# Optimization experiments

Measured on AMD Instinct MI355X. Metric: run time of the kernel, lower is better.

The kernel has to match this reference:

```python
import jax, jax.numpy as jnp
import numpy as np

HEADS = 8


def setup_inputs() -> dict:
    key = jax.random.key(0)
    ks = jax.random.split(key, 7)
    b, t, e, h = 4, 2048, 128, HEADS
    x = jax.random.normal(ks[0], (b, t, e), dtype=jnp.float32)
    mask = jax.random.randint(ks[1], (1, t, t), 0, 2, dtype=jnp.int32)
    Wq = jax.random.normal(ks[2], (e, e * h), dtype=jnp.float32) / np.sqrt(e)
    Wk = jax.random.normal(ks[3], (e, e * h), dtype=jnp.float32) / np.sqrt(e)
    Wv = jax.random.normal(ks[4], (e, e * h), dtype=jnp.float32) / np.sqrt(e)
    Wu = jax.random.normal(ks[5], (e * h, e), dtype=jnp.float32) / np.sqrt(e * h)
    bu = jax.random.normal(ks[6], (e,), dtype=jnp.float32) * 0.01
    return {"x": x, "mask": mask, "Wq": Wq, "Wk": Wk, "Wv": Wv, "Wu": Wu, "bu": bu}


def reference(x, mask, Wq, Wk, Wv, Wu, bu):
    b, t, e = x.shape
    h = HEADS
    scale = e ** (-0.25)  # original scales q and k each by e**(1/4)
    # project and split heads: (b, t, h, e) -> (b, h, t, e)
    q = (x @ Wq).reshape(b, t, h, e).transpose(0, 2, 1, 3) * scale
    k = (x @ Wk).reshape(b, t, h, e).transpose(0, 2, 1, 3) * scale
    v = (x @ Wv).reshape(b, t, h, e).transpose(0, 2, 1, 3)
    dot = jnp.einsum('bhqe,bhke->bhqk', q, k)  # (b, h, t, t)
    # causal mask: strictly-upper triangle set to -inf (mask_diagonal=False -> offset=1)
    causal = jnp.triu(jnp.ones((t, t), dtype=bool), k=1)
    dot = jnp.where(causal, jnp.float32(-np.inf), dot)
    # external mask: positions where mask == 0 set to -1e9 (broadcast over b*h)
    dot = jnp.where((mask == 0)[:, None, :, :], jnp.float32(-1e9), dot)
    att = jax.nn.softmax(dot, axis=-1)
    out = jnp.einsum('bhqk,bhke->bhqe', att, v)
    out = out.transpose(0, 2, 1, 3).reshape(b, t, h * e)
    return out @ Wu + bu
```

## Files before the change

kernel.cpp:

```cpp
#include <hip/hip_runtime.h>
#include <hip/hip_bf16.h>

typedef unsigned short u16;
typedef unsigned int u32;
typedef __attribute__((ext_vector_type(8))) short bf16x8;
typedef __attribute__((ext_vector_type(4))) float f32x4;
typedef __attribute__((ext_vector_type(8))) unsigned short u16x8;
typedef __attribute__((ext_vector_type(2))) unsigned int u32x2;

#define T_ 2048
#define H_ 8
#define BH_ 32
#define M_ 8192
#define SCALE_QK 0.29730177875068026f

__device__ __forceinline__ u16 f2bf(float f) {
  union { __hip_bfloat16 h; u16 u; } cv; cv.h = __float2bfloat16(f); return cv.u;
}
__device__ __forceinline__ float bf2f(u16 u) {
  union { u16 u; __hip_bfloat16 h; } cv; cv.u = u; return __bfloat162float(cv.h);
}


__global__ __launch_bounds__(256)
void prep_kernel(const float* __restrict__ x, const float* __restrict__ Wq,
                 const float* __restrict__ Wk, const float* __restrict__ Wv,
                 const float* __restrict__ Wu,
                 u16* __restrict__ xb, u16* __restrict__ WT, u16* __restrict__ WuT)
{
  int i = blockIdx.x * 256 + threadIdx.x;
  if (i < M_ * 128) { xb[i] = f2bf(x[i]); return; }
  int j = i - M_ * 128;
  if (j < 3072 * 128) {
    int n = j >> 7, k = j & 127;
    float w;
    if (n < 1024)      w = Wq[k * 1024 + n] * SCALE_QK;
    else if (n < 2048) w = Wk[k * 1024 + (n - 1024)] * SCALE_QK;
    else               w = Wv[k * 1024 + (n - 2048)];
    WT[j] = f2bf(w);
    return;
  }
  int u = j - 3072 * 128;
  if (u < 128 * 1024) {
    int n = u >> 10, k = u & 1023;
    WuT[u] = f2bf(Wu[k * 128 + n]);
  }
}

__global__ __launch_bounds__(256)
void maskprep_kernel(const int* __restrict__ mask, u32* __restrict__ mbits,
                     u32* __restrict__ deglist, u32* __restrict__ degcount,
                     float* __restrict__ cnt0inv)
{
  int wave = threadIdx.x >> 6, lane = threadIdx.x & 63;
  int q = blockIdx.x * 4 + wave;
  const int* row = mask + (long)q * 2048;
  unsigned long long anyvis = 0ull;
  int cnt1 = 0;
  for (int it = 0; it < 32; ++it) {
    int k = it * 64 + lane;
    unsigned long long bal = __ballot(row[k] != 0);
    if (lane == 0) {
      mbits[q * 64 + it * 2]     = (u32)bal;
      mbits[q * 64 + it * 2 + 1] = (u32)(bal >> 32);
    }
    cnt1 += __popcll(bal);
    int lim = q - it * 64;
    if (lim >= 63)      anyvis |= bal;
    else if (lim >= 0)  anyvis |= (bal & ((2ull << lim) - 1ull));
  }
  if (lane == 0) {
    int c0 = 2048 - cnt1;
    cnt0inv[q] = (c0 > 0) ? 1.0f / (float)c0 : 0.0f;
    if (anyvis == 0ull) {
      u32 slot = atomicAdd(degcount, 1u);
      deglist[slot] = (u32)q;
    }
  }
}

__global__ __launch_bounds__(256)
void qkv_kernel(const u16* __restrict__ xb, const u16* __restrict__ WT,
                u16* __restrict__ Qb, u16* __restrict__ Kimg, u16* __restrict__ Vimg)
{
  __shared__ __align__(16) u16 As[128 * 128];
  __shared__ __align__(16) u16 Bs[128 * 128];
  const int tid = threadIdx.x;
  const int n0 = blockIdx.x * 128;
  const int m0 = blockIdx.y * 128;
#pragma unroll
  for (int i = 0; i < 8; ++i) {
    int c = tid + 256 * i;
    int row = c >> 4, d0 = (c & 15) * 8;
    int soff = row * 128 + ((((d0 >> 3)) ^ (row & 15)) << 3);
    *(u16x8*)(&As[soff]) = *(const u16x8*)(&xb[(m0 + row) * 128 + d0]);
    *(u16x8*)(&Bs[soff]) = *(const u16x8*)(&WT[(n0 + row) * 128 + d0]);
  }
  __syncthreads();
  const int wave = tid >> 6, lane = tid & 63;
  const int lr = lane & 15, lg = lane >> 4;
  const int wm = (wave >> 1) * 64, wn = (wave & 1) * 64;
  f32x4 acc[4][4];
#pragma unroll
  for (int a = 0; a < 4; ++a)
#pragma unroll
    for (int b = 0; b < 4; ++b) acc[a][b] = (f32x4){0.f, 0.f, 0.f, 0.f};
#pragma unroll
  for (int ks = 0; ks < 4; ++ks) {
    bf16x8 af[4], bf[4];
#pragma unroll
    for (int mt = 0; mt < 4; ++mt) {
      int row = wm + mt * 16 + lr, chunk = lg + ks * 4;
      af[mt] = *(const bf16x8*)(&As[row * 128 + ((chunk ^ (row & 15)) << 3)]);
    }
#pragma unroll
    for (int nt = 0; nt < 4; ++nt) {
      int row = wn + nt * 16 + lr, chunk = lg + ks * 4;
      bf[nt] = *(const bf16x8*)(&Bs[row * 128 + ((chunk ^ (row & 15)) << 3)]);
    }
#pragma unroll
    for (int mt = 0; mt < 4; ++mt)
#pragma unroll
      for (int nt = 0; nt < 4; ++nt)
        acc[mt][nt] = __builtin_amdgcn_mfma_f32_16x16x32_bf16(af[mt], bf[nt], acc[mt][nt], 0, 0, 0);
  }
  const int mat = n0 >> 10;
  const int hh = (n0 & 1023) >> 7;
  const int bb = m0 >> 11;
  const long bhb = (long)(bb * H_ + hh);
  __syncthreads();
  if (mat != 2) {
#pragma unroll
    for (int mt = 0; mt < 4; ++mt)
#pragma unroll
      for (int nt = 0; nt < 4; ++nt)
#pragma unroll
        for (int r = 0; r < 4; ++r) {
          int tl = wm + mt * 16 + lg * 4 + r;
          int d  = wn + nt * 16 + lr;
          As[tl * 128 + ((((d >> 3)) ^ (tl & 15)) << 3) + (d & 7)] = f2bf(acc[mt][nt][r]);
        }
    __syncthreads();
    if (mat == 0) {
#pragma unroll
      for (int i = 0; i < 8; ++i) {
        int c = tid + 256 * i;
        int row = c >> 4, d0 = (c & 15) * 8;
        u16x8 v = *(const u16x8*)(&As[row * 128 + ((((d0 >> 3)) ^ (row & 15)) << 3)]);
        *(u16x8*)(&Qb[(bhb * T_ + ((m0 + row) & 2047)) * 128 + d0]) = v;
      }
    } else {
#pragma unroll
      for (int i = 0; i < 8; ++i) {
        int c = tid + 256 * i;
        int row = c >> 4, d0 = (c & 15) * 8;
        u16x8 v = *(const u16x8*)(&As[row * 128 + ((((d0 >> 3)) ^ (row & 15)) << 3)]);
        int t = (m0 + row) & 2047;
        int kt = t >> 6, kr = t & 63;
        *(u16x8*)(&Kimg[(bhb * 32 + kt) * 8192 + kr * 128 + ((((d0 >> 3)) ^ (kr & 15)) << 3)]) = v;
      }
    }
  } else {
    u16* TT = As;
#pragma unroll
    for (int mt = 0; mt < 4; ++mt)
#pragma unroll
      for (int nt = 0; nt < 4; ++nt)
#pragma unroll
        for (int r = 0; r < 4; ++r) {
          int tl = wm + mt * 16 + lg * 4 + r;
          int d  = wn + nt * 16 + lr;
          TT[d * 128 + ((((tl >> 3)) ^ (d & 15)) << 3) + (tl & 7)] = f2bf(acc[mt][nt][r]);
        }
    __syncthreads();
    const int tg0 = m0 & 2047;
#pragma unroll
    for (int i = 0; i < 8; ++i) {
      int c = tid + 256 * i;
      int d = c >> 4, t0 = (c & 15) * 8;
      u16x8 v = *(const u16x8*)(&TT[d * 128 + ((((t0 >> 3)) ^ (d & 15)) << 3)]);
      int tg = tg0 + t0;
      int kt = tg >> 6, kk = tg & 63;
      *(u16x8*)(&Vimg[(bhb * 32 + kt) * 8192 + d * 64 + (((kk >> 3) ^ (d & 7)) << 3)]) = v;
    }
  }
}

__global__ __launch_bounds__(256, 3)
void flash_kernel(const u16* __restrict__ Qb, const u16* __restrict__ Kimg,
                  const u16* __restrict__ Vimg, const u32* __restrict__ mbits,
                  u16* __restrict__ Ob)
{
  __shared__ __align__(16) u16 Ks[64 * 128];
  __shared__ __align__(16) u16 VTs[128 * 64];
  __shared__ __align__(16) u16 Ps[4][16 * 64];
  const int tid = threadIdx.x;
  const int qt = 31 - (blockIdx.x >> 5);
  const int bh = blockIdx.x & 31;
  const int q0 = qt * 64;
  const int wave = tid >> 6, lane = tid & 63;
  const int lr = lane & 15, lg = lane >> 4;
  const long base = (long)bh * T_ * 128;
  const long iblk = (long)bh * 32;
  const int ldsoff = wave * 2048 + lane * 8;
  const int qrl = wave * 16 + lr;
  const int swz = (lr & 7) << 1;

  bf16x8 qf[4];
  {
    const u16* qrow = Qb + base + (long)(q0 + qrl) * 128;
#pragma unroll
    for (int ks = 0; ks < 4; ++ks)
      qf[ks] = *(const bf16x8*)(&qrow[lg * 8 + ks * 32]);
  }
  f32x4 acc[8];
#pragma unroll
  for (int i = 0; i < 8; ++i) acc[i] = (f32x4){0.f, 0.f, 0.f, 0.f};
  float mrun = -__builtin_inff(), lrun = 0.f;

  u16x8 kreg[4], vreg[4];
  {
    const u16* ks0 = Kimg + iblk * 8192 + ldsoff;
    const u16* vs0 = Vimg + iblk * 8192 + ldsoff;
#pragma unroll
    for (int i = 0; i < 4; ++i) {
      kreg[i] = *(const u16x8*)(ks0 + i * 512);
      vreg[i] = *(const u16x8*)(vs0 + i * 512);
    }
  }

  for (int kt = 0; kt <= qt; ++kt) {
    __syncthreads();
#pragma unroll
    for (int i = 0; i < 4; ++i) {
      *(u16x8*)(&Ks[ldsoff + i * 512]) = kreg[i];
      *(u16x8*)(&VTs[ldsoff + i * 512]) = vreg[i];
    }
    __syncthreads();
    if (kt < qt) {
      const u16* ksn = Kimg + (iblk + kt + 1) * 8192 + ldsoff;
      const u16* vsn = Vimg + (iblk + kt + 1) * 8192 + ldsoff;
#pragma unroll
      for (int i = 0; i < 4; ++i) {
        kreg[i] = *(const u16x8*)(ksn + i * 512);
        vreg[i] = *(const u16x8*)(vsn + i * 512);
      }
    }
    u32 mw0, mw1;
    {
      const u32* mp = &mbits[(q0 + qrl) * 64 + kt * 2];
      mw0 = mp[0]; mw1 = mp[1];
    }

    f32x4 s[4];
    __builtin_amdgcn_s_setprio(1);
#pragma unroll
    for (int ft = 0; ft < 4; ++ft) {
      f32x4 sa = (f32x4){0.f, 0.f, 0.f, 0.f};
#pragma unroll
      for (int ks = 0; ks < 4; ++ks) {
        int kr = ft * 16 + lr, chunk = lg + ks * 4;
        bf16x8 kf = *(const bf16x8*)(&Ks[kr * 128 + ((chunk ^ (kr & 15)) << 3)]);
        sa = __builtin_amdgcn_mfma_f32_16x16x32_bf16(kf, qf[ks], sa, 0, 0, 0);
      }
      s[ft] = sa;
    }
    __builtin_amdgcn_s_setprio(0);
    const bool diag = (kt == qt);
#pragma unroll
    for (int ft = 0; ft < 4; ++ft) {
      u32 w = (ft & 2) ? mw1 : mw0;
      int kbase = ft * 16 + lg * 4;
      int sh = ((ft & 1) << 4) + lg * 4;
#pragma unroll
      for (int r = 0; r < 4; ++r) {
        bool vis = (w >> (sh + r)) & 1u;
        if (diag && (kbase + r) > qrl) vis = false;
        if (!vis) s[ft][r] = -__builtin_inff();
      }
    }
    float t0 = fmaxf(fmaxf(s[0][0], s[0][1]), fmaxf(s[0][2], s[0][3]));
    float t1 = fmaxf(fmaxf(s[1][0], s[1][1]), fmaxf(s[1][2], s[1][3]));
    float t2 = fmaxf(fmaxf(s[2][0], s[2][1]), fmaxf(s[2][2], s[2][3]));
    float t3 = fmaxf(fmaxf(s[3][0], s[3][1]), fmaxf(s[3][2], s[3][3]));
    float tm = fmaxf(fmaxf(t0, t1), fmaxf(t2, t3));
    tm = fmaxf(tm, __shfl_xor(tm, 16));
    tm = fmaxf(tm, __shfl_xor(tm, 32));
    float mnew = fmaxf(mrun, tm);
    float msafe = (mnew == -__builtin_inff()) ? 0.f : mnew;
    float fac = __expf(mrun - msafe);
    const bool grew = (mnew != mrun);
    mrun = mnew;
    float rs = 0.f;
#pragma unroll
    for (int ft = 0; ft < 4; ++ft) {
      float p0 = __expf(s[ft][0] - msafe), p1 = __expf(s[ft][1] - msafe);
      float p2 = __expf(s[ft][2] - msafe), p3 = __expf(s[ft][3] - msafe);
      s[ft][0] = p0; s[ft][1] = p1; s[ft][2] = p2; s[ft][3] = p3;
      rs += (p0 + p1) + (p2 + p3);
    }
    rs += __shfl_xor(rs, 16);
    rs += __shfl_xor(rs, 32);
    lrun = lrun * fac + rs;
    if (__any(grew)) {
#pragma unroll
      for (int nt = 0; nt < 8; ++nt)
#pragma unroll
        for (int r = 0; r < 4; ++r) acc[nt][r] *= fac;
    }
#pragma unroll
    for (int ft = 0; ft < 4; ++ft) {
      u16 h0 = f2bf(s[ft][0]), h1 = f2bf(s[ft][1]);
      u16 h2 = f2bf(s[ft][2]), h3 = f2bf(s[ft][3]);
      u32x2 pw; pw[0] = (u32)h0 | ((u32)h1 << 16); pw[1] = (u32)h2 | ((u32)h3 << 16);
      int ch4 = (ft * 4 + lg) ^ swz;
      *(u32x2*)(&Ps[wave][lr * 64 + ch4 * 4]) = pw;
    }
    bf16x8 pa[2];
#pragma unroll
    for (int s2 = 0; s2 < 2; ++s2) {
      int ch4b = (s2 * 8 + lg * 2) ^ swz;
      pa[s2] = *(const bf16x8*)(&Ps[wave][lr * 64 + ch4b * 4]);
    }
    __builtin_amdgcn_s_setprio(1);
#pragma unroll
    for (int nt = 0; nt < 8; ++nt)
#pragma unroll
      for (int s2 = 0; s2 < 2; ++s2) {
        int d = nt * 16 + lr, chunk = lg + s2 * 4;
        bf16x8 vf = *(const bf16x8*)(&VTs[d * 64 + ((chunk ^ (d & 7)) << 3)]);
        acc[nt] = __builtin_amdgcn_mfma_f32_16x16x32_bf16(vf, pa[s2], acc[nt], 0, 0, 0);
      }
    __builtin_amdgcn_s_setprio(0);
  }
  const float inv = (lrun > 0.f) ? 1.f / lrun : 0.f;
  const long orow = base + (long)(q0 + qrl) * 128;
#pragma unroll
  for (int nt = 0; nt < 8; ++nt) {
    u16 h0 = f2bf(acc[nt][0] * inv), h1 = f2bf(acc[nt][1] * inv);
    u16 h2 = f2bf(acc[nt][2] * inv), h3 = f2bf(acc[nt][3] * inv);
    u32x2 ow; ow[0] = (u32)h0 | ((u32)h1 << 16); ow[1] = (u32)h2 | ((u32)h3 << 16);
    *(u32x2*)(&Ob[orow + nt * 16 + lg * 4]) = ow;
  }
}

__global__ __launch_bounds__(256)
void fixup_partial_kernel(const u32* __restrict__ deglist, const u32* __restrict__ degcount,
                          const u32* __restrict__ mbits, const u16* __restrict__ Vimg,
                          float* __restrict__ partial)
{
  const int slot = blockIdx.z;
  const u32 cnt = *degcount;
  if (slot >= (int)cnt) return;
  const int ksec = blockIdx.x, bh = blockIdx.y;
  const int q = (int)deglist[slot];
  const int t = threadIdx.x;
  const int d = t & 127, kc = t >> 7;
  const u16* vb = Vimg + ((long)bh * 32 + ksec) * 8192 + d * 64;
  const u32 w0 = mbits[q * 64 + ksec * 2];
  const u32 w1 = mbits[q * 64 + ksec * 2 + 1];
  float a = 0.f;
#pragma unroll
  for (int i = 0; i < 4; ++i) {
    int c = kc * 4 + i;
    u32 bits = ((kc == 0) ? (w0 >> (c * 8)) : (w1 >> ((c - 4) * 8))) & 0xffu;
    u16x8 v = *(const u16x8*)(&vb[(c ^ (d & 7)) << 3]);
#pragma unroll
    for (int j = 0; j < 8; ++j)
      a += ((bits >> j) & 1u) ? 0.f : bf2f(v[j]);
  }
  __shared__ float tmp[2][128];
  tmp[kc][d] = a;
  __syncthreads();
  if (t < 128)
    partial[(((long)slot * BH_ + bh) * 128 + d) * 32 + ksec] = tmp[0][d] + tmp[1][d];
}

__global__ __launch_bounds__(128)
void fixup_combine_kernel(const u32* __restrict__ deglist, const u32* __restrict__ degcount,
                          const float* __restrict__ cnt0inv, const float* __restrict__ partial,
                          u16* __restrict__ Ob)
{
  const int slot = blockIdx.x;
  const u32 cnt = *degcount;
  if (slot >= (int)cnt) return;
  const int bh = blockIdx.y;
  const int q = (int)deglist[slot];
  const int d = threadIdx.x;
  const float* p = partial + (((long)slot * BH_ + bh) * 128 + d) * 32;
  float s = 0.f;
#pragma unroll
  for (int i = 0; i < 8; ++i) {
    f32x4 v = *(const f32x4*)(&p[i * 4]);
    s += (v[0] + v[1]) + (v[2] + v[3]);
  }
  Ob[((long)bh * T_ + q) * 128 + d] = f2bf(s * cnt0inv[q]);
}

__global__ __launch_bounds__(256)
void fixup_slow_kernel(const u32* __restrict__ deglist, const u32* __restrict__ degcount,
                       const float* __restrict__ cnt0inv, const u32* __restrict__ mbits,
                       const u16* __restrict__ Vimg, u16* __restrict__ Ob)
{
  const u32 cnt = *degcount;
  const int bh = blockIdx.y;
  const int d = threadIdx.x & 127, half = threadIdx.x >> 7;
  __shared__ float tmp[2][128];
  const u16* vb = Vimg + (long)bh * 32 * 8192;
  for (u32 idx = 8 + blockIdx.x; idx < cnt; idx += gridDim.x) {
    const int q = (int)deglist[idx];
    const float inv = cnt0inv[q];
    float a = 0.f;
#pragma unroll 16
    for (int i = 0; i < 128; ++i) {
      int k0 = half * 1024 + i * 8;
      u32 w = mbits[q * 64 + (k0 >> 5)];
      u32 bits = (w >> (k0 & 31)) & 0xffu;
      int kt = k0 >> 6, kk = k0 & 63;
      u16x8 v = *(const u16x8*)(&vb[(long)kt * 8192 + d * 64 + (((kk >> 3) ^ (d & 7)) << 3)]);
#pragma unroll
      for (int j = 0; j < 8; ++j)
        a += ((bits >> j) & 1u) ? 0.f : bf2f(v[j]);
    }
    tmp[half][d] = a;
    __syncthreads();
    if (half == 0)
      Ob[((long)bh * T_ + q) * 128 + d] = f2bf((tmp[0][d] + tmp[1][d]) * inv);
    __syncthreads();
  }
}

__global__ __launch_bounds__(256)
void outproj_kernel(const u16* __restrict__ Ob, const u16* __restrict__ WuT,
                    const float* __restrict__ bu, float* __restrict__ out)
{
  __shared__ __align__(16) u16 As[32 * 128];
  __shared__ __align__(16) u16 Bs[128 * 128];
  const int tid = threadIdx.x;
  const int m0 = blockIdx.x * 32;
  const int wave = tid >> 6, lane = tid & 63;
  const int lr = lane & 15, lg = lane >> 4;
  f32x4 acc[2][2];
#pragma unroll
  for (int a = 0; a < 2; ++a)
#pragma unroll
    for (int b = 0; b < 2; ++b) acc[a][b] = (f32x4){0.f, 0.f, 0.f, 0.f};
  for (int kc = 0; kc < 8; ++kc) {
    __syncthreads();
#pragma unroll
    for (int i = 0; i < 2; ++i) {
      int c = tid + 256 * i;
      int row = c >> 4, d0 = (c & 15) * 8;
      int m = m0 + row, bb = m >> 11, t = m & 2047;
      *(u16x8*)(&As[row * 128 + ((((d0 >> 3)) ^ (row & 15)) << 3)]) =
          *(const u16x8*)(&Ob[((long)(bb * H_ + kc) * T_ + t) * 128 + d0]);
    }
#pragma unroll
    for (int i = 0; i < 8; ++i) {
      int c = tid + 256 * i;
      int row = c >> 4, d0 = (c & 15) * 8;
      *(u16x8*)(&Bs[row * 128 + ((((d0 >> 3)) ^ (row & 15)) << 3)]) =
          *(const u16x8*)(&WuT[row * 1024 + kc * 128 + d0]);
    }
    __syncthreads();
#pragma unroll
    for (int ks = 0; ks < 4; ++ks) {
      bf16x8 af[2], bf2[2];
#pragma unroll
      for (int mt = 0; mt < 2; ++mt) {
        int row = mt * 16 + lr, chunk = lg + ks * 4;
        af[mt] = *(const bf16x8*)(&As[row * 128 + ((chunk ^ (row & 15)) << 3)]);
      }
#pragma unroll
      for (int nt = 0; nt < 2; ++nt) {
        int row = wave * 32 + nt * 16 + lr, chunk = lg + ks * 4;
        bf2[nt] = *(const bf16x8*)(&Bs[row * 128 + ((chunk ^ (row & 15)) << 3)]);
      }
#pragma unroll
      for (int mt = 0; mt < 2; ++mt)
#pragma unroll
        for (int nt = 0; nt < 2; ++nt)
          acc[mt][nt] = __builtin_amdgcn_mfma_f32_16x16x32_bf16(af[mt], bf2[nt], acc[mt][nt], 0, 0, 0);
    }
  }
#pragma unroll
  for (int mt = 0; mt < 2; ++mt)
#pragma unroll
    for (int nt = 0; nt < 2; ++nt) {
      int n = wave * 32 + nt * 16 + lr;
      float bias = bu[n];
#pragma unroll
      for (int r = 0; r < 4; ++r) {
        int m = m0 + mt * 16 + lg * 4 + r;
        out[(long)m * 128 + n] = acc[mt][nt][r] + bias;
      }
    }
}

extern "C" void kernel_launch(void* const* d_in, const int* in_sizes, int n_in,
                              void* d_out, int out_size, void* d_ws, size_t ws_size,
                              hipStream_t stream)
{
  (void)in_sizes; (void)n_in; (void)out_size; (void)ws_size;
  const float* x   = (const float*)d_in[0];
  const int*   msk = (const int*)d_in[1];
  const float* Wq  = (const float*)d_in[2];
  const float* Wk  = (const float*)d_in[3];
  const float* Wv  = (const float*)d_in[4];
  const float* Wu  = (const float*)d_in[5];
  const float* bu  = (const float*)d_in[6];
  float* out = (float*)d_out;

  u16* Qb   = (u16*)d_ws;
  u16* Kimg = Qb + (size_t)BH_ * T_ * 128;
  u16* Vimg = Kimg + (size_t)BH_ * T_ * 128;
  u16* Obf  = Vimg + (size_t)BH_ * T_ * 128;
  u16* xb   = Obf + (size_t)BH_ * T_ * 128;
  u16* WT   = xb + (size_t)M_ * 128;
  u16* WuT  = WT + (size_t)3072 * 128;
  u32* mbits   = (u32*)(WuT + (size_t)128 * 1024);
  u32* deglist = mbits + (size_t)2048 * 64;
  u32* degcount = deglist + 2048;
  float* cnt0inv = (float*)(degcount + 1);
  float* partial = (float*)Qb;

  hipMemsetAsync(degcount, 0, sizeof(u32), stream);
  prep_kernel<<<6144, 256, 0, stream>>>(x, Wq, Wk, Wv, Wu, xb, WT, WuT);
  maskprep_kernel<<<512, 256, 0, stream>>>(msk, mbits, deglist, degcount, cnt0inv);
  qkv_kernel<<<dim3(24, 64), 256, 0, stream>>>(xb, WT, Qb, Kimg, Vimg);
  flash_kernel<<<1024, 256, 0, stream>>>(Qb, Kimg, Vimg, mbits, Obf);
  fixup_partial_kernel<<<dim3(32, 32, 8), 256, 0, stream>>>(deglist, degcount, mbits, Vimg, partial);
  fixup_combine_kernel<<<dim3(8, 32), 128, 0, stream>>>(deglist, degcount, cnt0inv, partial, Obf);
  fixup_slow_kernel<<<dim3(32, 32), 256, 0, stream>>>(deglist, degcount, cnt0inv, mbits, Vimg, Obf);
  outproj_kernel<<<256, 256, 0, stream>>>(Obf, WuT, bu, out);
}
```

Before: 135.8 us.

## Use 128-row query tiles with 32x32 MFMA and register-shuffled P operands

The flash kernel now handles 128 query rows per block (32 per wave) and uses 32x32x16 bf16 MFMA for both QK^T and PV, which doubles reuse of each K/V tile loaded into LDS. The probability matrix is repacked into MFMA operands with cross-lane shuffles instead of a round trip through LDS, and the output is staged through LDS for coalesced 16-byte stores. Query-tile scheduling is changed to interleave heavy and light causal tiles. The cost is more registers per thread (occupancy hint lowered from 3 to 2 blocks) and half as many blocks, which may leave the device underfilled.

Measured after the change: 179.0 us. 31.8% more time.

```diff
diff --git a/kernel.cpp b/kernel.cpp
--- a/kernel.cpp
+++ b/kernel.cpp
@@ -5,6 +5,7 @@
 typedef unsigned int u32;
 typedef __attribute__((ext_vector_type(8))) short bf16x8;
 typedef __attribute__((ext_vector_type(4))) float f32x4;
+typedef __attribute__((ext_vector_type(16))) float f32x16;
 typedef __attribute__((ext_vector_type(8))) unsigned short u16x8;
 typedef __attribute__((ext_vector_type(2))) unsigned int u32x2;
 
@@ -186,36 +187,39 @@
   }
 }
 
-__global__ __launch_bounds__(256, 3)
+__global__ __launch_bounds__(256, 2)
 void flash_kernel(const u16* __restrict__ Qb, const u16* __restrict__ Kimg,
                   const u16* __restrict__ Vimg, const u32* __restrict__ mbits,
                   u16* __restrict__ Ob)
 {
-  __shared__ __align__(16) u16 Ks[64 * 128];
-  __shared__ __align__(16) u16 VTs[128 * 64];
-  __shared__ __align__(16) u16 Ps[4][16 * 64];
+  __shared__ __align__(16) u16 SMEM[128 * 128];
+  u16* const Ks  = SMEM;
+  u16* const VTs = SMEM + 8192;
   const int tid = threadIdx.x;
-  const int qt = 31 - (blockIdx.x >> 5);
+  const int idx = blockIdx.x >> 5;
+  const int qt = (idx < 8) ? (15 - idx) : (idx - 8);
   const int bh = blockIdx.x & 31;
-  const int q0 = qt * 64;
+  const int q0 = qt * 128;
   const int wave = tid >> 6, lane = tid & 63;
-  const int lr = lane & 15, lg = lane >> 4;
+  const int l31 = lane & 31, h = lane >> 5;
   const long base = (long)bh * T_ * 128;
   const long iblk = (long)bh * 32;
   const int ldsoff = wave * 2048 + lane * 8;
-  const int qrl = wave * 16 + lr;
-  const int swz = (lr & 7) << 1;
-
-  bf16x8 qf[4];
+  const int qrl = wave * 32 + l31;
+  const int nkv = 2 * (qt + 1);
+
+  bf16x8 qf[8];
   {
-    const u16* qrow = Qb + base + (long)(q0 + qrl) * 128;
-#pragma unroll
-    for (int ks = 0; ks < 4; ++ks)
-      qf[ks] = *(const bf16x8*)(&qrow[lg * 8 + ks * 32]);
-  }
-  f32x4 acc[8];
-#pragma unroll
-  for (int i = 0; i < 8; ++i) acc[i] = (f32x4){0.f, 0.f, 0.f, 0.f};
+    const u16* qrow = Qb + base + (long)(q0 + qrl) * 128 + h * 8;
+#pragma unroll
+    for (int st = 0; st < 8; ++st)
+      qf[st] = *(const bf16x8*)(&qrow[st * 16]);
+  }
+  f32x16 acc[4];
+#pragma unroll
+  for (int i = 0; i < 4; ++i)
+#pragma unroll
+    for (int r = 0; r < 16; ++r) acc[i][r] = 0.f;
   float mrun = -__builtin_inff(), lrun = 0.f;
 
   u16x8 kreg[4], vreg[4];
@@ -229,7 +233,7 @@
     }
   }
 
-  for (int kt = 0; kt <= qt; ++kt) {
+  for (int kt = 0; kt < nkv; ++kt) {
     __syncthreads();
 #pragma unroll
     for (int i = 0; i < 4; ++i) {
@@ -237,7 +241,7 @@
       *(u16x8*)(&VTs[ldsoff + i * 512]) = vreg[i];
     }
     __syncthreads();
-    if (kt < qt) {
+    if (kt + 1 < nkv) {
       const u16* ksn = Kimg + (iblk + kt + 1) * 8192 + ldsoff;
       const u16* vsn = Vimg + (iblk + kt + 1) * 8192 + ldsoff;
 #pragma unroll
@@ -252,95 +256,139 @@
       mw0 = mp[0]; mw1 = mp[1];
     }
 
-    f32x4 s[4];
+    f32x16 s[2];
+#pragma unroll
+    for (int k2 = 0; k2 < 2; ++k2)
+#pragma unroll
+      for (int r = 0; r < 16; ++r) s[k2][r] = 0.f;
     __builtin_amdgcn_s_setprio(1);
 #pragma unroll
-    for (int ft = 0; ft < 4; ++ft) {
-      f32x4 sa = (f32x4){0.f, 0.f, 0.f, 0.f};
-#pragma unroll
-      for (int ks = 0; ks < 4; ++ks) {
-        int kr = ft * 16 + lr, chunk = lg + ks * 4;
-        bf16x8 kf = *(const bf16x8*)(&Ks[kr * 128 + ((chunk ^ (kr & 15)) << 3)]);
-        sa = __builtin_amdgcn_mfma_f32_16x16x32_bf16(kf, qf[ks], sa, 0, 0, 0);
-      }
-      s[ft] = sa;
+    for (int k2 = 0; k2 < 2; ++k2) {
+      const int key = k2 * 32 + l31;
+      const int swk = (key & 15);
+#pragma unroll
+      for (int st = 0; st < 8; ++st) {
+        int chunk = 2 * st + h;
+        bf16x8 kf = *(const bf16x8*)(&Ks[key * 128 + ((chunk ^ swk) << 3)]);
+        s[k2] = __builtin_amdgcn_mfma_f32_32x32x16_bf16(kf, qf[st], s[k2], 0, 0, 0);
+      }
     }
     __builtin_amdgcn_s_setprio(0);
-    const bool diag = (kt == qt);
-#pragma unroll
-    for (int ft = 0; ft < 4; ++ft) {
-      u32 w = (ft & 2) ? mw1 : mw0;
-      int kbase = ft * 16 + lg * 4;
-      int sh = ((ft & 1) << 4) + lg * 4;
-#pragma unroll
-      for (int r = 0; r < 4; ++r) {
-        bool vis = (w >> (sh + r)) & 1u;
-        if (diag && (kbase + r) > qrl) vis = false;
-        if (!vis) s[ft][r] = -__builtin_inff();
-      }
-    }
-    float t0 = fmaxf(fmaxf(s[0][0], s[0][1]), fmaxf(s[0][2], s[0][3]));
-    float t1 = fmaxf(fmaxf(s[1][0], s[1][1]), fmaxf(s[1][2], s[1][3]));
-    float t2 = fmaxf(fmaxf(s[2][0], s[2][1]), fmaxf(s[2][2], s[2][3]));
-    float t3 = fmaxf(fmaxf(s[3][0], s[3][1]), fmaxf(s[3][2], s[3][3]));
-    float tm = fmaxf(fmaxf(t0, t1), fmaxf(t2, t3));
-    tm = fmaxf(tm, __shfl_xor(tm, 16));
+
+    const bool diag = (kt >= 2 * qt);
+    const int kv0 = kt * 64;
+#pragma unroll
+    for (int k2 = 0; k2 < 2; ++k2) {
+      u32 w = k2 ? mw1 : mw0;
+#pragma unroll
+      for (int r = 0; r < 16; ++r) {
+        int bitpos = (r & 3) + 8 * (r >> 2) + 4 * h;
+        bool vis = (w >> bitpos) & 1u;
+        if (diag && (kv0 + k2 * 32 + bitpos) > (q0 + qrl)) vis = false;
+        if (!vis) s[k2][r] = -__builtin_inff();
+      }
+    }
+    float tv[8];
+#pragma unroll
+    for (int i = 0; i < 8; ++i)
+      tv[i] = fmaxf(fmaxf(s[i >> 2][(i & 3) * 4 + 0], s[i >> 2][(i & 3) * 4 + 1]),
+                    fmaxf(s[i >> 2][(i & 3) * 4 + 2], s[i >> 2][(i & 3) * 4 + 3]));
+    float tm = fmaxf(fmaxf(fmaxf(tv[0], tv[1]), fmaxf(tv[2], tv[3])),
+                     fmaxf(fmaxf(tv[4], tv[5]), fmaxf(tv[6], tv[7])));
     tm = fmaxf(tm, __shfl_xor(tm, 32));
     float mnew = fmaxf(mrun, tm);
     float msafe = (mnew == -__builtin_inff()) ? 0.f : mnew;
     float fac = __expf(mrun - msafe);
     const bool grew = (mnew != mrun);
     mrun = mnew;
-    float rs = 0.f;
-#pragma unroll
-    for (int ft = 0; ft < 4; ++ft) {
-      float p0 = __expf(s[ft][0] - msafe), p1 = __expf(s[ft][1] - msafe);
-      float p2 = __expf(s[ft][2] - msafe), p3 = __expf(s[ft][3] - msafe);
-      s[ft][0] = p0; s[ft][1] = p1; s[ft][2] = p2; s[ft][3] = p3;
-      rs += (p0 + p1) + (p2 + p3);
-    }
-    rs += __shfl_xor(rs, 16);
+    float rs0 = 0.f, rs1 = 0.f, rs2 = 0.f, rs3 = 0.f;
+#pragma unroll
+    for (int k2 = 0; k2 < 2; ++k2)
+#pragma unroll
+      for (int g = 0; g < 4; ++g) {
+        float p0 = __expf(s[k2][4 * g + 0] - msafe);
+        float p1 = __expf(s[k2][4 * g + 1] - msafe);
+        float p2 = __expf(s[k2][4 * g + 2] - msafe);
+        float p3 = __expf(s[k2][4 * g + 3] - msafe);
+        s[k2][4 * g + 0] = p0; s[k2][4 * g + 1] = p1;
+        s[k2][4 * g + 2] = p2; s[k2][4 * g + 3] = p3;
+        rs0 += p0; rs1 += p1; rs2 += p2; rs3 += p3;
+      }
+    float rs = (rs0 + rs1) + (rs2 + rs3);
     rs += __shfl_xor(rs, 32);
     lrun = lrun * fac + rs;
     if (__any(grew)) {
 #pragma unroll
-      for (int nt = 0; nt < 8; ++nt)
-#pragma unroll
-        for (int r = 0; r < 4; ++r) acc[nt][r] *= fac;
-    }
-#pragma unroll
-    for (int ft = 0; ft < 4; ++ft) {
-      u16 h0 = f2bf(s[ft][0]), h1 = f2bf(s[ft][1]);
-      u16 h2 = f2bf(s[ft][2]), h3 = f2bf(s[ft][3]);
-      u32x2 pw; pw[0] = (u32)h0 | ((u32)h1 << 16); pw[1] = (u32)h2 | ((u32)h3 << 16);
-      int ch4 = (ft * 4 + lg) ^ swz;
-      *(u32x2*)(&Ps[wave][lr * 64 + ch4 * 4]) = pw;
-    }
-    bf16x8 pa[2];
-#pragma unroll
-    for (int s2 = 0; s2 < 2; ++s2) {
-      int ch4b = (s2 * 8 + lg * 2) ^ swz;
-      pa[s2] = *(const bf16x8*)(&Ps[wave][lr * 64 + ch4b * 4]);
+      for (int dt = 0; dt < 4; ++dt)
+#pragma unroll
+        for (int r = 0; r < 16; ++r) acc[dt][r] *= fac;
+    }
+    u32x2 grp[2][4];
+#pragma unroll
+    for (int k2 = 0; k2 < 2; ++k2)
+#pragma unroll
+      for (int g = 0; g < 4; ++g) {
+        u16 b0 = f2bf(s[k2][4 * g + 0]), b1 = f2bf(s[k2][4 * g + 1]);
+        u16 b2 = f2bf(s[k2][4 * g + 2]), b3 = f2bf(s[k2][4 * g + 3]);
+        grp[k2][g][0] = (u32)b0 | ((u32)b1 << 16);
+        grp[k2][g][1] = (u32)b2 | ((u32)b3 << 16);
+      }
+    u32x2 rcv[2][2];
+#pragma unroll
+    for (int k2 = 0; k2 < 2; ++k2)
+#pragma unroll
+      for (int e = 0; e < 2; ++e) {
+        u32x2 snd = h ? grp[k2][e * 2] : grp[k2][e * 2 + 1];
+        rcv[k2][e][0] = (u32)__shfl_xor((int)snd[0], 32);
+        rcv[k2][e][1] = (u32)__shfl_xor((int)snd[1], 32);
+      }
+    bf16x8 pa[4];
+#pragma unroll
+    for (int s4 = 0; s4 < 4; ++s4) {
+      int k2 = s4 >> 1, e = s4 & 1;
+      u32x2 own = grp[k2][e * 2 + h];
+      u32x2 rc = rcv[k2][e];
+      union { u32 u[4]; bf16x8 v; } cv;
+      cv.u[0] = h ? rc[0] : own[0];
+      cv.u[1] = h ? rc[1] : own[1];
+      cv.u[2] = h ? own[0] : rc[0];
+      cv.u[3] = h ? own[1] : rc[1];
+      pa[s4] = cv.v;
     }
     __builtin_amdgcn_s_setprio(1);
 #pragma unroll
-    for (int nt = 0; nt < 8; ++nt)
-#pragma unroll
-      for (int s2 = 0; s2 < 2; ++s2) {
-        int d = nt * 16 + lr, chunk = lg + s2 * 4;
-        bf16x8 vf = *(const bf16x8*)(&VTs[d * 64 + ((chunk ^ (d & 7)) << 3)]);
-        acc[nt] = __builtin_amdgcn_mfma_f32_16x16x32_bf16(vf, pa[s2], acc[nt], 0, 0, 0);
-      }
+    for (int dt = 0; dt < 4; ++dt) {
+      const int d = dt * 32 + l31;
+      const int swd = (d & 7);
+#pragma unroll
+      for (int s4 = 0; s4 < 4; ++s4) {
+        int chunk = 2 * s4 + h;
+        bf16x8 vf = *(const bf16x8*)(&VTs[d * 64 + ((chunk ^ swd) << 3)]);
+        acc[dt] = __builtin_amdgcn_mfma_f32_32x32x16_bf16(vf, pa[s4], acc[dt], 0, 0, 0);
+      }
+    }
     __builtin_amdgcn_s_setprio(0);
   }
   const float inv = (lrun > 0.f) ? 1.f / lrun : 0.f;
-  const long orow = base + (long)(q0 + qrl) * 128;
-#pragma unroll
-  for (int nt = 0; nt < 8; ++nt) {
-    u16 h0 = f2bf(acc[nt][0] * inv), h1 = f2bf(acc[nt][1] * inv);
-    u16 h2 = f2bf(acc[nt][2] * inv), h3 = f2bf(acc[nt][3] * inv);
-    u32x2 ow; ow[0] = (u32)h0 | ((u32)h1 << 16); ow[1] = (u32)h2 | ((u32)h3 << 16);
-    *(u32x2*)(&Ob[orow + nt * 16 + lg * 4]) = ow;
+  __syncthreads();
+  const int swzr = (qrl & 15) << 3;
+#pragma unroll
+  for (int dt = 0; dt < 4; ++dt)
+#pragma unroll
+    for (int g = 0; g < 4; ++g) {
+      int d0 = dt * 32 + g * 8 + h * 4;
+      u16 a0 = f2bf(acc[dt][4 * g + 0] * inv), a1 = f2bf(acc[dt][4 * g + 1] * inv);
+      u16 a2 = f2bf(acc[dt][4 * g + 2] * inv), a3 = f2bf(acc[dt][4 * g + 3] * inv);
+      u32x2 pw; pw[0] = (u32)a0 | ((u32)a1 << 16); pw[1] = (u32)a2 | ((u32)a3 << 16);
+      *(u32x2*)(&SMEM[qrl * 128 + (d0 ^ swzr)]) = pw;
+    }
+  __syncthreads();
+#pragma unroll
+  for (int i = 0; i < 8; ++i) {
+    int c = tid + 256 * i;
+    int row = c >> 4, d0 = (c & 15) * 8;
+    u16x8 v = *(const u16x8*)(&SMEM[row * 128 + (d0 ^ ((row & 15) << 3))]);
+    *(u16x8*)(&Ob[base + (long)(q0 + row) * 128 + d0]) = v;
   }
 }
 
@@ -528,7 +576,7 @@
   prep_kernel<<<6144, 256, 0, stream>>>(x, Wq, Wk, Wv, Wu, xb, WT, WuT);
   maskprep_kernel<<<512, 256, 0, stream>>>(msk, mbits, deglist, degcount, cnt0inv);
   qkv_kernel<<<dim3(24, 64), 256, 0, stream>>>(xb, WT, Qb, Kimg, Vimg);
-  flash_kernel<<<1024, 256, 0, stream>>>(Qb, Kimg, Vimg, mbits, Obf);
+  flash_kernel<<<512, 256, 0, stream>>>(Qb, Kimg, Vimg, mbits, Obf);
   fixup_partial_kernel<<<dim3(32, 32, 8), 256, 0, stream>>>(deglist, degcount, mbits, Vimg, partial);
   fixup_combine_kernel<<<dim3(8, 32), 128, 0, stream>>>(deglist, degcount, cnt0inv, partial, Obf);
   fixup_slow_kernel<<<dim3(32, 32), 256, 0, stream>>>(deglist, degcount, cnt0inv, mbits, Vimg, Obf);
```
